# Kernel optimization log

Hardware: AMD Instinct MI355X
Metric: run time of the kernel (lower is better)

## Reference

```python
import jax, jax.numpy as jnp
import numpy as np

T = 4194304  # sequence length (2**22)

def setup_inputs() -> dict:
    key = jax.random.key(0)
    k = jax.random.split(key, 7)
    return {
        "x_0": jax.random.normal(k[0], (1, 2), dtype=jnp.float32),
        "u": jax.random.normal(k[1], (2, T), dtype=jnp.float32),
        "timedelta": jax.random.uniform(k[2], (T,), dtype=jnp.float32),
        # scale W_A down so the linear recurrence x_t = A x_{t-1} + ... is stable over 4M steps
        "W_A": 0.3 * jax.random.normal(k[3], (2, 2), dtype=jnp.float32),
        "b_A": 0.1 * jax.random.normal(k[4], (2,), dtype=jnp.float32),
        "W_B": jax.random.normal(k[5], (2, 2), dtype=jnp.float32),
        "b_B": 0.1 * jax.random.normal(k[6], (2,), dtype=jnp.float32),
    }

def reference(x_0, u, timedelta, W_A, b_A, W_B, b_B):
    # forward_PINN: linear state recurrence x_t = A x_{t-1} + B u_t (+biases),
    # output_t = physics_prediction(x_{t-1}, u_t, dt_t) - x_t
    x0 = x_0[0]          # [2] state (x, y)
    u_seq = u.T          # [T, 2] controls (speed, heading)

    def step(x_prev, inp):
        u_t, dt = inp                                  # [2], scalar
        x_t = W_A @ x_prev + b_A + W_B @ u_t + b_B     # [2]
        c = u_t[0] * dt
        pinn = x_prev + jnp.stack([c * jnp.cos(u_t[1]), c * jnp.sin(u_t[1])])
        return x_t, pinn - x_t

    _, x_out = jax.lax.scan(step, x0, (u_seq, timedelta))  # [T, 2]
    return x_out
```

## Files before the change

### kernel.cpp

```cpp
#include <hip/hip_runtime.h>

#define T_TOTAL 4194304
#define S 16
#define WIN 1024
#define NWIN 2
#define WAVE_T (WIN * NWIN)
#define NTHREADS 256
#define WAVES_PB (NTHREADS / 64)
#define BLOCK_T (WAVE_T * WAVES_PB)

struct M22 { float m00, m01, m10, m11; };
__device__ __forceinline__ M22 mmul(const M22& X, const M22& Y) {
    M22 r;
    r.m00 = fmaf(X.m00, Y.m00, X.m01 * Y.m10);
    r.m01 = fmaf(X.m00, Y.m01, X.m01 * Y.m11);
    r.m10 = fmaf(X.m10, Y.m00, X.m11 * Y.m10);
    r.m11 = fmaf(X.m10, Y.m01, X.m11 * Y.m11);
    return r;
}

struct alignas(16) F16 { float f[16]; };
__device__ __forceinline__ void load16(F16& d, const float* __restrict__ p) {
    const float4* q = (const float4*)p;
    float4 a0 = q[0], a1 = q[1], a2 = q[2], a3 = q[3];
    *(float4*)&d.f[0]  = a0;
    *(float4*)&d.f[4]  = a1;
    *(float4*)&d.f[8]  = a2;
    *(float4*)&d.f[12] = a3;
}

__global__ __launch_bounds__(NTHREADS)
void pinn_rnn_kernel(const float* __restrict__ x0p,
                     const float* __restrict__ u,
                     const float* __restrict__ td,
                     const float* __restrict__ WA,
                     const float* __restrict__ bA,
                     const float* __restrict__ WB,
                     const float* __restrict__ bB,
                     float* __restrict__ out)
{
    const int lane = threadIdx.x & 63;
    const int gw   = blockIdx.x * WAVES_PB + (threadIdx.x >> 6);
    const int b0   = gw * WAVE_T;
    const int b1   = b0 + WIN;
    const bool first = (gw == 0);

    const float a00 = WA[0], a01 = WA[1], a10 = WA[2], a11 = WA[3];
    const float w00 = WB[0], w01 = WB[1], w10 = WB[2], w11 = WB[3];
    const float bc0 = bA[0] + bB[0];
    const float bc1 = bA[1] + bB[1];
    const float X0 = x0p[0], X1 = x0p[1];

    const float* u0 = u;
    const float* u1 = u + T_TOTAL;

    const int t0 = b0 + lane * S;
    F16 U0a, U1a, DTa;
    load16(U0a, u0 + t0);
    load16(U1a, u1 + t0);
    load16(DTa, td + t0);

    F16 H0 = {}, H1 = {};
    if (lane < 4 && !first) {
        const int th = b0 - 64 + lane * S;
        load16(H0, u0 + th);
        load16(H1, u1 + th);
    }

    M22 A   = { a00, a01, a10, a11 };
    M22 A2  = mmul(A,  A );
    M22 A4  = mmul(A2, A2);
    M22 A8  = mmul(A4, A4);
    M22 M   = mmul(A8, A8);
    M22 M2_ = mmul(M,  M );
    M22 M3_ = mmul(M2_, M);

    auto zsr = [&](const F16& P0, const F16& P1, float& cx, float& cy) {
        float x0v = 0.f, x1v = 0.f;
        #pragma unroll
        for (int j = 0; j < S; ++j) {
            float v0 = fmaf(w00, P0.f[j], fmaf(w01, P1.f[j], bc0));
            float v1 = fmaf(w10, P0.f[j], fmaf(w11, P1.f[j], bc1));
            float n0 = fmaf(a00, x0v, fmaf(a01, x1v, v0));
            float n1 = fmaf(a10, x0v, fmaf(a11, x1v, v1));
            x0v = n0; x1v = n1;
        }
        cx = x0v; cy = x1v;
    };

    auto prefix = [&](float cx, float cy, float xw0, float xw1,
                      float& xi0, float& xi1) {
        float s0 = 0.f, s1 = 0.f, tx, ty;
        tx = __shfl_up(cx, 1); ty = __shfl_up(cy, 1);
        if (lane >= 1) { s0 += tx; s1 += ty; }
        tx = __shfl_up(cx, 2); ty = __shfl_up(cy, 2);
        if (lane >= 2) { s0 += fmaf(M.m00, tx, M.m01 * ty);
                         s1 += fmaf(M.m10, tx, M.m11 * ty); }
        tx = __shfl_up(cx, 3); ty = __shfl_up(cy, 3);
        if (lane >= 3) { s0 += fmaf(M2_.m00, tx, M2_.m01 * ty);
                         s1 += fmaf(M2_.m10, tx, M2_.m11 * ty); }
        tx = __shfl_up(cx, 4); ty = __shfl_up(cy, 4);
        if (lane >= 4) { s0 += fmaf(M3_.m00, tx, M3_.m01 * ty);
                         s1 += fmaf(M3_.m10, tx, M3_.m11 * ty); }
        if (lane < 4) {
            M22 P;
            if      (lane == 0) P = { 1.f, 0.f, 0.f, 1.f };
            else if (lane == 1) P = M;
            else if (lane == 2) P = M2_;
            else                P = M3_;
            s0 += fmaf(P.m00, xw0, P.m01 * xw1);
            s1 += fmaf(P.m10, xw0, P.m11 * xw1);
        }
        xi0 = s0; xi1 = s1;
    };

    auto replay = [&](const F16& P0, const F16& P1, const F16& PD,
                      float xi0, float xi1, int base,
                      float& xo0, float& xo1) {
        float x0v = xi0, x1v = xi1;
        float4* og = (float4*)out + (base >> 1) + lane * (S / 2);
        #pragma unroll
        for (int p = 0; p < S / 2; ++p) {
            float o[4];
            #pragma unroll
            for (int q = 0; q < 2; ++q) {
                int j = 2 * p + q;
                float v0 = fmaf(w00, P0.f[j], fmaf(w01, P1.f[j], bc0));
                float v1 = fmaf(w10, P0.f[j], fmaf(w11, P1.f[j], bc1));
                float n0 = fmaf(a00, x0v, fmaf(a01, x1v, v0));
                float n1 = fmaf(a10, x0v, fmaf(a11, x1v, v1));
                float cc = P0.f[j] * PD.f[j];
                float sn, cs;
                __sincosf(P1.f[j], &sn, &cs);
                o[2 * q]     = fmaf(cc, cs, x0v) - n0;
                o[2 * q + 1] = fmaf(cc, sn, x1v) - n1;
                x0v = n0; x1v = n1;
            }
            og[p] = make_float4(o[0], o[1], o[2], o[3]);
        }
        xo0 = x0v; xo1 = x1v;
    };

    float cx, cy;
    zsr(U0a, U1a, cx, cy);

    const int t1 = b1 + lane * S;
    F16 U0b, U1b, DTb;
    load16(U0b, u0 + t1);
    load16(U1b, u1 + t1);
    load16(DTb, td + t1);

    float xw0, xw1;
    if (first) {
        xw0 = X0; xw1 = X1;
    } else {
        float hcx, hcy;
        zsr(H0, H1, hcx, hcy);
        float h0x = __shfl(hcx, 0), h0y = __shfl(hcy, 0);
        float h1x = __shfl(hcx, 1), h1y = __shfl(hcy, 1);
        float h2x = __shfl(hcx, 2), h2y = __shfl(hcy, 2);
        float h3x = __shfl(hcx, 3), h3y = __shfl(hcy, 3);
        xw0 = h3x + fmaf(M.m00, h2x, M.m01 * h2y)
                  + fmaf(M2_.m00, h1x, M2_.m01 * h1y)
                  + fmaf(M3_.m00, h0x, M3_.m01 * h0y);
        xw1 = h3y + fmaf(M.m10, h2x, M.m11 * h2y)
                  + fmaf(M2_.m10, h1x, M2_.m11 * h1y)
                  + fmaf(M3_.m10, h0x, M3_.m11 * h0y);
    }

    float xi0, xi1, xf0, xf1;
    prefix(cx, cy, xw0, xw1, xi0, xi1);
    replay(U0a, U1a, DTa, xi0, xi1, b0, xf0, xf1);

    float cw0 = __shfl(xf0, 63);
    float cw1 = __shfl(xf1, 63);

    zsr(U0b, U1b, cx, cy);
    prefix(cx, cy, cw0, cw1, xi0, xi1);
    replay(U0b, U1b, DTb, xi0, xi1, b1, xf0, xf1);
}

extern "C" void kernel_launch(void* const* d_in, const int* in_sizes, int n_in,
                              void* d_out, int out_size, void* d_ws, size_t ws_size,
                              hipStream_t stream) {
    const float* x0p = (const float*)d_in[0];
    const float* u   = (const float*)d_in[1];
    const float* td  = (const float*)d_in[2];
    const float* WA  = (const float*)d_in[3];
    const float* bA  = (const float*)d_in[4];
    const float* WB  = (const float*)d_in[5];
    const float* bB  = (const float*)d_in[6];
    float* outp = (float*)d_out;

    dim3 grid(T_TOTAL / BLOCK_T);
    dim3 block(NTHREADS);
    pinn_rnn_kernel<<<grid, block, 0, stream>>>(x0p, u, td, WA, bA, WB, bB, outp);
}
```

Measured before the change: 115.2 us.

## Stage outputs through swizzled LDS for coalesced stores and hoist second-window loads

Each wave now writes its per-lane output pairs into a per-wave LDS buffer, using an XOR swizzle to limit bank conflicts. It then reads the buffer back so that consecutive lanes issue consecutive float4 global stores, replacing the lane-strided 64-byte-apart store pattern. The loads for the second window are also moved ahead of the first window's compute so their latency is better hidden. A min-blocks hint of 2 is added to launch bounds. In exchange the kernel uses 32 KB of LDS per block, adds extra LDS traffic, and relies on in-wave ordering of LDS accesses without a barrier.

```diff
diff --git a/kernel.cpp b/kernel.cpp
--- a/kernel.cpp
+++ b/kernel.cpp
@@ -29,7 +29,7 @@
     *(float4*)&d.f[12] = a3;
 }
 
-__global__ __launch_bounds__(NTHREADS)
+__global__ __launch_bounds__(NTHREADS, 2)
 void pinn_rnn_kernel(const float* __restrict__ x0p,
                      const float* __restrict__ u,
                      const float* __restrict__ td,
@@ -39,8 +39,11 @@
                      const float* __restrict__ bB,
                      float* __restrict__ out)
 {
+    __shared__ float2 lout[WAVES_PB * WIN];
+
     const int lane = threadIdx.x & 63;
-    const int gw   = blockIdx.x * WAVES_PB + (threadIdx.x >> 6);
+    const int wid  = threadIdx.x >> 6;
+    const int gw   = blockIdx.x * WAVES_PB + wid;
     const int b0   = gw * WAVE_T;
     const int b1   = b0 + WIN;
     const bool first = (gw == 0);
@@ -66,6 +69,12 @@
         load16(H0, u0 + th);
         load16(H1, u1 + th);
     }
+
+    const int t1 = b1 + lane * S;
+    F16 U0b, U1b, DTb;
+    load16(U0b, u0 + t1);
+    load16(U1b, u1 + t1);
+    load16(DTb, td + t1);
 
     M22 A   = { a00, a01, a10, a11 };
     M22 A2  = mmul(A,  A );
@@ -114,41 +123,40 @@
         xi0 = s0; xi1 = s1;
     };
 
-    auto replay = [&](const F16& P0, const F16& P1, const F16& PD,
-                      float xi0, float xi1, int base,
-                      float& xo0, float& xo1) {
+    auto replay_store = [&](const F16& P0, const F16& P1, const F16& PD,
+                            float xi0, float xi1, int base,
+                            float& xo0, float& xo1) {
+        float2* lw   = lout + wid * WIN;
+        float2* lrow = lw + lane * S;
+        const int xm = lane & 14;
         float x0v = xi0, x1v = xi1;
-        float4* og = (float4*)out + (base >> 1) + lane * (S / 2);
         #pragma unroll
-        for (int p = 0; p < S / 2; ++p) {
-            float o[4];
-            #pragma unroll
-            for (int q = 0; q < 2; ++q) {
-                int j = 2 * p + q;
-                float v0 = fmaf(w00, P0.f[j], fmaf(w01, P1.f[j], bc0));
-                float v1 = fmaf(w10, P0.f[j], fmaf(w11, P1.f[j], bc1));
-                float n0 = fmaf(a00, x0v, fmaf(a01, x1v, v0));
-                float n1 = fmaf(a10, x0v, fmaf(a11, x1v, v1));
-                float cc = P0.f[j] * PD.f[j];
-                float sn, cs;
-                __sincosf(P1.f[j], &sn, &cs);
-                o[2 * q]     = fmaf(cc, cs, x0v) - n0;
-                o[2 * q + 1] = fmaf(cc, sn, x1v) - n1;
-                x0v = n0; x1v = n1;
-            }
-            og[p] = make_float4(o[0], o[1], o[2], o[3]);
+        for (int j = 0; j < S; ++j) {
+            float v0 = fmaf(w00, P0.f[j], fmaf(w01, P1.f[j], bc0));
+            float v1 = fmaf(w10, P0.f[j], fmaf(w11, P1.f[j], bc1));
+            float n0 = fmaf(a00, x0v, fmaf(a01, x1v, v0));
+            float n1 = fmaf(a10, x0v, fmaf(a11, x1v, v1));
+            float cc = P0.f[j] * PD.f[j];
+            float sn, cs;
+            __sincosf(P1.f[j], &sn, &cs);
+            lrow[j ^ xm] = make_float2(fmaf(cc, cs, x0v) - n0,
+                                       fmaf(cc, sn, x1v) - n1);
+            x0v = n0; x1v = n1;
         }
         xo0 = x0v; xo1 = x1v;
+        const float4* lo4 = (const float4*)lw;
+        float4* og = (float4*)out + (base >> 1);
+        #pragma unroll
+        for (int m = 0; m < 8; ++m) {
+            int f    = m * 64 + lane;
+            int i0   = f << 1;
+            int slot = i0 ^ ((i0 >> 4) & 14);
+            og[f] = lo4[slot >> 1];
+        }
     };
 
     float cx, cy;
     zsr(U0a, U1a, cx, cy);
-
-    const int t1 = b1 + lane * S;
-    F16 U0b, U1b, DTb;
-    load16(U0b, u0 + t1);
-    load16(U1b, u1 + t1);
-    load16(DTb, td + t1);
 
     float xw0, xw1;
     if (first) {
@@ -170,14 +178,14 @@
 
     float xi0, xi1, xf0, xf1;
     prefix(cx, cy, xw0, xw1, xi0, xi1);
-    replay(U0a, U1a, DTa, xi0, xi1, b0, xf0, xf1);
+    replay_store(U0a, U1a, DTa, xi0, xi1, b0, xf0, xf1);
 
     float cw0 = __shfl(xf0, 63);
     float cw1 = __shfl(xf1, 63);
 
     zsr(U0b, U1b, cx, cy);
     prefix(cx, cy, cw0, cw1, xi0, xi1);
-    replay(U0b, U1b, DTb, xi0, xi1, b1, xf0, xf1);
+    replay_store(U0b, U1b, DTb, xi0, xi1, b1, xf0, xf1);
 }
 
 extern "C" void kernel_launch(void* const* d_in, const int* in_sizes, int n_in,
```

Measured after the change: 111.2 us. 1.04x faster.
